# Kernel optimization log

Hardware: AMD Instinct MI355X
Metric: run time of the kernel (lower is better)

Reference implementation:

```python
import jax, jax.numpy as jnp
import numpy as np

B = 2; GH = 64; GW = 64
D = 384; H = 12; HD = D // H          # head dim 32
SD = 2                                 # spatial dims
KS = 7; ST = 3; PAD = (KS - 1) // 2    # strided conv params
RR = 0.5
NROT = (int(HD * RR) // (2 * SD)) * (2 * SD)   # 16 rotated dims per head
PAIRS = NROT // (2 * SD)                        # 4 freq pairs per spatial axis
ITERS = 3
BASE = 10000.0
LN_EPS = 1e-5
EPS = np.float32(1.1920929e-07)        # torch.finfo(float32).eps


def setup_inputs() -> dict:
    key = jax.random.key(0)
    ks = jax.random.split(key, 8)
    s = 0.02
    # base rotary frequencies with 'sqrt' scaling, per head/axis, + init jitter
    inv = BASE ** (-jnp.arange(PAIRS, dtype=jnp.float32) / PAIRS)
    inv = jnp.sqrt(inv)
    rose_freqs = jnp.broadcast_to(inv, (H, SD, PAIRS)) + 0.02 * jax.random.normal(ks[7], (H, SD, PAIRS), jnp.float32)
    return {
        "x": jax.random.normal(ks[0], (B, GH * GW, D), jnp.float32),
        "conv_w": jax.random.normal(ks[1], (D, D, KS, KS), jnp.float32) / np.float32(np.sqrt(D * KS * KS)),
        "conv_b": jnp.zeros((D,), jnp.float32),
        "kv_w": s * jax.random.normal(ks[2], (D, 2 * D), jnp.float32),
        "kv_b": jnp.zeros((2 * D,), jnp.float32),
        "q_w": s * jax.random.normal(ks[3], (D, D), jnp.float32),
        "q_b": jnp.zeros((D,), jnp.float32),
        "mlp_w1": s * jax.random.normal(ks[4], (D, 4 * D), jnp.float32),
        "mlp_b1": jnp.zeros((4 * D,), jnp.float32),
        "mlp_w2": s * jax.random.normal(ks[5], (4 * D, D), jnp.float32),
        "mlp_b2": jnp.zeros((D,), jnp.float32),
        "g1": jnp.ones((D,), jnp.float32), "b1": jnp.zeros((D,), jnp.float32),
        "g2": jnp.ones((D,), jnp.float32), "b2": jnp.zeros((D,), jnp.float32),
        "g3": jnp.ones((D,), jnp.float32), "b3": jnp.zeros((D,), jnp.float32),
        "temp": jnp.array([1.0 / np.sqrt(D)], jnp.float32),
        "rose_freqs": rose_freqs,
        "grid_h": GH,
        "grid_w": GW,
    }


def _ln(x, g, b):
    mu = jnp.mean(x, axis=-1, keepdims=True)
    var = jnp.mean(jnp.square(x - mu), axis=-1, keepdims=True)
    return (x - mu) * jax.lax.rsqrt(var + LN_EPS) * g + b


def _rose(x, freqs, grid_shape, spacing):
    """Rotary spatial embedding. x: (B, N, D) -> (B, H, N, HD) with first NROT
    head dims rotated by per-head learnable frequencies over real-space coords."""
    Bx, N, _ = x.shape
    axes = [jnp.arange(g, dtype=jnp.float32) * sp for g, sp in zip(grid_shape, spacing)]
    coords = jnp.stack(jnp.meshgrid(*axes, indexing='ij'), axis=-1).reshape(-1, SD)  # (N, SD)
    ang = jnp.einsum('ns,hsp->hnsp', coords, freqs).reshape(H, N, NROT // 2)
    cos = jnp.cos(ang)[None]; sin = jnp.sin(ang)[None]                # (1,H,N,NROT/2)
    xh = x.reshape(Bx, N, H, HD).transpose(0, 2, 1, 3)                # (B,H,N,HD)
    x1 = xh[..., 0:NROT:2]; x2 = xh[..., 1:NROT:2]
    rot = jnp.stack([x1 * cos - x2 * sin, x1 * sin + x2 * cos], axis=-1).reshape(Bx, H, N, NROT)
    return jnp.concatenate([rot, xh[..., NROT:]], axis=-1)


def reference(x, conv_w, conv_b, kv_w, kv_b, q_w, q_b, mlp_w1, mlp_b1, mlp_w2, mlp_b2,
              g1, b1, g2, b2, g3, b3, temp, rose_freqs, grid_h, grid_w):
    in_grid = (int(grid_h), int(grid_w)); in_sp = (1.0, 1.0)
    q_grid = tuple((g + 2 * PAD - KS) // ST + 1 for g in in_grid)
    q_sp = tuple(s * ST for s in in_sp)
    Bx, N_in, _ = x.shape
    N_out = q_grid[0] * q_grid[1]

    # strided conv producing low-res slots, then norm1
    xt = x.transpose(0, 2, 1).reshape(Bx, D, *in_grid)
    xo = jax.lax.conv_general_dilated(xt, conv_w, (ST, ST), [(PAD, PAD), (PAD, PAD)])
    xo = xo + conv_b[None, :, None, None]
    x_out = _ln(xo.reshape(Bx, D, N_out).transpose(0, 2, 1), g1, b1)  # (B,N_out,D)

    attn_q = attn_k = None
    for _ in range(ITERS):
        kv = x @ kv_w + kv_b
        k_lin, v = kv[..., :D], kv[..., D:]
        k = temp * _rose(k_lin, rose_freqs, in_grid, in_sp)           # (B,H,N_in,HD)
        q = _rose(x_out @ q_w + q_b, rose_freqs, q_grid, q_sp)       # (B,H,N_out,HD)
        # concrete attn: softmax over keys of q.k^T (temp already folded into k)
        attn_k = jax.nn.softmax(jnp.einsum('bhqd,bhkd->bhqk', q, k), axis=-1)
        attn_q = attn_k / (jnp.sum(attn_k, axis=-2, keepdims=True) + EPS)
        vh = v.reshape(Bx, N_in, H, HD).transpose(0, 2, 1, 3)
        upd = jnp.einsum('bhqk,bhkd->bhqd', attn_q, vh).transpose(0, 2, 1, 3).reshape(Bx, N_out, D)
        x_out = x_out + _ln(upd, g2, b2)
        h = jax.nn.gelu(x_out @ mlp_w1 + mlp_b1, approximate=False) @ mlp_w2 + mlp_b2
        x_out = x_out + _ln(h, g3, b3)
    return x_out, attn_q, attn_k
```

## Files before the change

### kernel.cpp

```cpp
#include <hip/hip_runtime.h>
#include <math.h>

#define BB 2
#define D_ 384
#define H_ 12
#define HD 32
#define NIN 4096
#define NOUT 484
#define MOUT (BB*NOUT)
#define MIN_ (BB*NIN)
#define QW_ 22
#define CK 18816
#define NSLICE 49
#define LN_EPS 1e-5f
#define EPS_ 1.1920929e-07f

typedef short bf16x8 __attribute__((ext_vector_type(8)));
typedef float f32x4  __attribute__((ext_vector_type(4)));

__device__ __forceinline__ unsigned f2bf(float f){
  unsigned u = __float_as_uint(f);
  u += 0x7fffu + ((u>>16)&1u);
  return u>>16;
}

static const size_t OXOUT = 0;
static const size_t OKB   = 371712;
static const size_t OVH   = OKB + 1572864;
static const size_t OQB   = OVH + 3145728;
static const size_t OQP   = OQB + 196608;
static const size_t OL0   = OQP + 371712;
static const size_t OCS   = OL0 + 12288;
static const size_t OLP   = OCS + 98304;
static const size_t OUPD  = OLP + 196608;
static const size_t OH1   = OUPD + 371712;
static const size_t OH2   = OH1 + 1486848;
static const size_t OQWB  = OH2 + 1486848;
static const size_t OW1B  = OQWB + 73728;
static const size_t OW2B  = OW1B + 294912;

__global__ __launch_bounds__(256)
void packxk(const float* __restrict__ x, ushort* __restrict__ xb){
  int i = blockIdx.x*256 + threadIdx.x;
  int base = i*4;
  if (base >= MIN_*D_) return;
  float4 v = *(const float4*)(x + base);
  uint2 o;
  o.x = f2bf(v.x) | (f2bf(v.y)<<16);
  o.y = f2bf(v.z) | (f2bf(v.w)<<16);
  *(uint2*)(xb + base) = o;
}

__global__ __launch_bounds__(256)
void wtk2(const float* __restrict__ cw, ushort* __restrict__ wtb){
  int i = blockIdx.x*256 + threadIdx.x;
  if (i >= CK*D_) return;
  int n = i / CK;
  int r = i - n*CK;
  int di = r/49, kyx = r - di*49;
  wtb[((size_t)kyx*D_ + n)*D_ + di] = (ushort)f2bf(cw[i]);
}

__global__ __launch_bounds__(256)
void packwk(const float* __restrict__ w, ushort* __restrict__ wb, int K, int N){
  int i = blockIdx.x*256 + threadIdx.x;
  if (i >= K*N) return;
  int k = i / N, n = i - k*N;
  wb[(size_t)n*K + k] = (ushort)f2bf(w[i]);
}

__global__ __launch_bounds__(256)
void convm(const ushort* __restrict__ xb, const ushort* __restrict__ wtb,
           float* __restrict__ part){
  __shared__ ushort As[128][40];
  __shared__ ushort Bs[128][40];
  const int t  = threadIdx.x;
  const int m0 = blockIdx.x*128, n0 = blockIdx.y*128, z = blockIdx.z;
  const int ky = z/7, kx = z - ky*7;
  const int r = t>>1, half = t&1;
  const int m = m0 + r;
  const int mq = (m < MOUT) ? m : 0;
  const int bbv = mq/NOUT, qq = mq - bbv*NOUT;
  const int oy = qq/QW_, ox = qq - oy*QW_;
  const int iy = oy*3-3+ky, ix = ox*3-3+kx;
  const bool aval = (m<MOUT) && iy>=0 && iy<64 && ix>=0 && ix<64;
  const ushort* asrc = xb + ((size_t)bbv*NIN + (aval ? iy*64+ix : 0))*D_ + half*16;
  const ushort* bsrc = wtb + ((size_t)z*D_ + n0 + r)*D_ + half*16;

  const int wv = t>>6;
  const int wr = (wv>>1)*64, wc = (wv&1)*64;
  const int ln = t&15, lq = (t>>4)&3;

  f32x4 acc[4][4];
#pragma unroll
  for (int i=0;i<4;i++)
#pragma unroll
    for (int j=0;j<4;j++) acc[i][j] = (f32x4){0.f,0.f,0.f,0.f};

  for (int dk=0; dk<D_; dk+=32){
    uint4 a0 = {0,0,0,0}, a1 = {0,0,0,0};
    if (aval){ a0 = *(const uint4*)(asrc+dk); a1 = *(const uint4*)(asrc+dk+8); }
    uint4 b0 = *(const uint4*)(bsrc+dk), b1 = *(const uint4*)(bsrc+dk+8);
    *(uint4*)&As[r][half*16]   = a0;  *(uint4*)&As[r][half*16+8] = a1;
    *(uint4*)&Bs[r][half*16]   = b0;  *(uint4*)&Bs[r][half*16+8] = b1;
    __syncthreads();
    bf16x8 af[4], bfr[4];
#pragma unroll
    for (int i=0;i<4;i++) af[i]  = *(const bf16x8*)&As[wr+i*16+ln][lq*8];
#pragma unroll
    for (int j=0;j<4;j++) bfr[j] = *(const bf16x8*)&Bs[wc+j*16+ln][lq*8];
#pragma unroll
    for (int i=0;i<4;i++)
#pragma unroll
      for (int j=0;j<4;j++)
        acc[i][j] = __builtin_amdgcn_mfma_f32_16x16x32_bf16(af[i], bfr[j], acc[i][j], 0,0,0);
    __syncthreads();
  }
#pragma unroll
  for (int i=0;i<4;i++){
    int rowb = m0 + wr + i*16 + lq*4;
#pragma unroll
    for (int j=0;j<4;j++){
      int col = n0 + wc + j*16 + ln;
#pragma unroll
      for (int rg=0; rg<4; rg++){
        int row = rowb + rg;
        if (row < MOUT) part[((size_t)z*MOUT + row)*D_ + col] = acc[i][j][rg];
      }
    }
  }
}

template<int ACT, bool ABF>
__global__ __launch_bounds__(256)
void gemmm(const void* __restrict__ Ain, const ushort* __restrict__ Wb,
           const float* __restrict__ bias, float* __restrict__ C,
           int M, int N, int K){
  __shared__ ushort As[128][40];
  __shared__ ushort Bs[128][40];
  const int t  = threadIdx.x;
  const int m0 = blockIdx.x*128, n0 = blockIdx.y*128;
  const int r = t>>1, half = t&1;
  const int m = m0 + r;
  const bool aval = (m < M);
  const float*  af32 = (const float*)Ain  + (size_t)(aval?m:0)*K + half*16;
  const ushort* ab16 = (const ushort*)Ain + (size_t)(aval?m:0)*K + half*16;
  const ushort* bsrc = Wb + (size_t)(n0 + r)*K + half*16;

  const int wv = t>>6;
  const int wr = (wv>>1)*64, wc = (wv&1)*64;
  const int ln = t&15, lq = (t>>4)&3;

  f32x4 acc[4][4];
#pragma unroll
  for (int i=0;i<4;i++)
#pragma unroll
    for (int j=0;j<4;j++) acc[i][j] = (f32x4){0.f,0.f,0.f,0.f};

  for (int dk=0; dk<K; dk+=32){
    uint4 a0 = {0,0,0,0}, a1 = {0,0,0,0};
    if (aval){
      if (ABF){
        a0 = *(const uint4*)(ab16+dk); a1 = *(const uint4*)(ab16+dk+8);
      } else {
        float4 f0 = *(const float4*)(af32+dk),   f1 = *(const float4*)(af32+dk+4);
        float4 f2 = *(const float4*)(af32+dk+8), f3 = *(const float4*)(af32+dk+12);
        a0.x = f2bf(f0.x)|(f2bf(f0.y)<<16); a0.y = f2bf(f0.z)|(f2bf(f0.w)<<16);
        a0.z = f2bf(f1.x)|(f2bf(f1.y)<<16); a0.w = f2bf(f1.z)|(f2bf(f1.w)<<16);
        a1.x = f2bf(f2.x)|(f2bf(f2.y)<<16); a1.y = f2bf(f2.z)|(f2bf(f2.w)<<16);
        a1.z = f2bf(f3.x)|(f2bf(f3.y)<<16); a1.w = f2bf(f3.z)|(f2bf(f3.w)<<16);
      }
    }
    uint4 b0 = *(const uint4*)(bsrc+dk), b1 = *(const uint4*)(bsrc+dk+8);
    *(uint4*)&As[r][half*16]   = a0;  *(uint4*)&As[r][half*16+8] = a1;
    *(uint4*)&Bs[r][half*16]   = b0;  *(uint4*)&Bs[r][half*16+8] = b1;
    __syncthreads();
    bf16x8 af[4], bfr[4];
#pragma unroll
    for (int i=0;i<4;i++) af[i]  = *(const bf16x8*)&As[wr+i*16+ln][lq*8];
#pragma unroll
    for (int j=0;j<4;j++) bfr[j] = *(const bf16x8*)&Bs[wc+j*16+ln][lq*8];
#pragma unroll
    for (int i=0;i<4;i++)
#pragma unroll
      for (int j=0;j<4;j++)
        acc[i][j] = __builtin_amdgcn_mfma_f32_16x16x32_bf16(af[i], bfr[j], acc[i][j], 0,0,0);
    __syncthreads();
  }
#pragma unroll
  for (int i=0;i<4;i++){
    int rowb = m0 + wr + i*16 + lq*4;
#pragma unroll
    for (int j=0;j<4;j++){
      int col = n0 + wc + j*16 + ln;
      float bv = bias[col];
#pragma unroll
      for (int rg=0; rg<4; rg++){
        int row = rowb + rg;
        if (row < M){
          float v = acc[i][j][rg] + bv;
          if (ACT==1) v = 0.5f*v*(1.f + erff(v*0.7071067811865475f));
          C[(size_t)row*N + col] = v;
        }
      }
    }
  }
}

__global__ __launch_bounds__(256)
void gemmsk(const float* __restrict__ Ain, const ushort* __restrict__ Wb,
            float* __restrict__ part){
  __shared__ ushort As[128][40];
  __shared__ ushort Bs[128][40];
  const int t  = threadIdx.x;
  const int m0 = blockIdx.x*128, n0 = blockIdx.y*128, z = blockIdx.z;
  const int r = t>>1, half = t&1;
  const int m = m0 + r;
  const bool aval = (m < MOUT);
  const float*  af32 = Ain + (size_t)(aval?m:0)*1536 + z*384 + half*16;
  const ushort* bsrc = Wb + (size_t)(n0 + r)*1536 + z*384 + half*16;

  const int wv = t>>6;
  const int wr = (wv>>1)*64, wc = (wv&1)*64;
  const int ln = t&15, lq = (t>>4)&3;

  f32x4 acc[4][4];
#pragma unroll
  for (int i=0;i<4;i++)
#pragma unroll
    for (int j=0;j<4;j++) acc[i][j] = (f32x4){0.f,0.f,0.f,0.f};

  for (int dk=0; dk<384; dk+=32){
    uint4 a0 = {0,0,0,0}, a1 = {0,0,0,0};
    if (aval){
      float4 f0 = *(const float4*)(af32+dk),   f1 = *(const float4*)(af32+dk+4);
      float4 f2 = *(const float4*)(af32+dk+8), f3 = *(const float4*)(af32+dk+12);
      a0.x = f2bf(f0.x)|(f2bf(f0.y)<<16); a0.y = f2bf(f0.z)|(f2bf(f0.w)<<16);
      a0.z = f2bf(f1.x)|(f2bf(f1.y)<<16); a0.w = f2bf(f1.z)|(f2bf(f1.w)<<16);
      a1.x = f2bf(f2.x)|(f2bf(f2.y)<<16); a1.y = f2bf(f2.z)|(f2bf(f2.w)<<16);
      a1.z = f2bf(f3.x)|(f2bf(f3.y)<<16); a1.w = f2bf(f3.z)|(f2bf(f3.w)<<16);
    }
    uint4 b0 = *(const uint4*)(bsrc+dk), b1 = *(const uint4*)(bsrc+dk+8);
    *(uint4*)&As[r][half*16]   = a0;  *(uint4*)&As[r][half*16+8] = a1;
    *(uint4*)&Bs[r][half*16]   = b0;  *(uint4*)&Bs[r][half*16+8] = b1;
    __syncthreads();
    bf16x8 af[4], bfr[4];
#pragma unroll
    for (int i=0;i<4;i++) af[i]  = *(const bf16x8*)&As[wr+i*16+ln][lq*8];
#pragma unroll
    for (int j=0;j<4;j++) bfr[j] = *(const bf16x8*)&Bs[wc+j*16+ln][lq*8];
#pragma unroll
    for (int i=0;i<4;i++)
#pragma unroll
      for (int j=0;j<4;j++)
        acc[i][j] = __builtin_amdgcn_mfma_f32_16x16x32_bf16(af[i], bfr[j], acc[i][j], 0,0,0);
    __syncthreads();
  }
#pragma unroll
  for (int i=0;i<4;i++){
    int rowb = m0 + wr + i*16 + lq*4;
#pragma unroll
    for (int j=0;j<4;j++){
      int col = n0 + wc + j*16 + ln;
#pragma unroll
      for (int rg=0; rg<4; rg++){
        int row = rowb + rg;
        if (row < MOUT) part[((size_t)z*MOUT + row)*D_ + col] = acc[i][j][rg];
      }
    }
  }
}

__device__ __forceinline__ float block_sum_384(float v){
  __shared__ float red[6];
#pragma unroll
  for (int o=32;o>0;o>>=1) v += __shfl_down(v,o);
  const int lane = threadIdx.x & 63, w = threadIdx.x >> 6;
  __syncthreads();
  if (lane==0) red[w] = v;
  __syncthreads();
  return red[0]+red[1]+red[2]+red[3]+red[4]+red[5];
}

template<int MODE>
__global__ __launch_bounds__(384)
void lnk(const float* __restrict__ in, const float* __restrict__ cb,
         const float* __restrict__ gg, const float* __restrict__ bb,
         float* __restrict__ xout){
  const int m = blockIdx.x, d = threadIdx.x;
  float v;
  if (MODE==0){
    v = cb[d];
    for (int z=0; z<NSLICE; z++) v += in[((size_t)z*MOUT + m)*D_ + d];
  } else if (MODE==1){
    int b = m/NOUT, q = m - b*NOUT;
    int h = d>>5, dd2 = d&31;
    v = in[(((size_t)(b*H_ + h))*NOUT + q)*HD + dd2];
  } else if (MODE==2){
    v = in[(size_t)m*D_ + d];
  } else {
    v = cb[d];
#pragma unroll
    for (int z=0; z<4; z++) v += in[((size_t)z*MOUT + m)*D_ + d];
  }
  float mu  = block_sum_384(v) * (1.f/D_);
  float ce  = v - mu;
  float var = block_sum_384(ce*ce) * (1.f/D_);
  float o = ce * rsqrtf(var + LN_EPS) * gg[d] + bb[d];
  float* dst = xout + (size_t)m*D_ + d;
  if (MODE==0) *dst = o;
  else *dst += o;
}

__global__ __launch_bounds__(256)
void rosek(const float* __restrict__ kvbuf, const float* __restrict__ rf,
           const float* __restrict__ temp,
           ushort* __restrict__ kb, float* __restrict__ vhb){
  int idx = blockIdx.x*256 + threadIdx.x;
  if (idx >= BB*H_*NIN) return;
  int n  = idx & (NIN-1);
  int bh = idx >> 12;
  int h  = bh % H_;
  int b  = bh / H_;
  float T = temp[0];
  int iy = n >> 6, ix = n & 63;
  const float* src = kvbuf + ((size_t)b*NIN + n)*768 + h*HD;
  float xv[HD];
#pragma unroll
  for (int d4=0; d4<8; d4++){
    float4 v = *(const float4*)(src + d4*4);
    xv[d4*4]=v.x; xv[d4*4+1]=v.y; xv[d4*4+2]=v.z; xv[d4*4+3]=v.w;
  }
  float out[HD];
#pragma unroll
  for (int tp=0; tp<8; tp++){
    int s2 = tp >> 2, p2 = tp & 3;
    float coord = (s2==0) ? (float)iy : (float)ix;
    float ang = coord * rf[(h*2+s2)*4 + p2];
    float sn, cn; sincosf(ang, &sn, &cn);
    float x1 = xv[2*tp], x2 = xv[2*tp+1];
    out[2*tp]   = x1*cn - x2*sn;
    out[2*tp+1] = x1*sn + x2*cn;
  }
#pragma unroll
  for (int d=16; d<HD; d++) out[d] = xv[d];
  ushort* dk = kb + ((size_t)bh*NIN + n)*HD;
#pragma unroll
  for (int g=0; g<4; g++){
    uint4 o;
    o.x = f2bf(T*out[g*8+0]) | (f2bf(T*out[g*8+1])<<16);
    o.y = f2bf(T*out[g*8+2]) | (f2bf(T*out[g*8+3])<<16);
    o.z = f2bf(T*out[g*8+4]) | (f2bf(T*out[g*8+5])<<16);
    o.w = f2bf(T*out[g*8+6]) | (f2bf(T*out[g*8+7])<<16);
    *(uint4*)(dk + g*8) = o;
  }
  const float* vs = src + D_;
  float* dv = vhb + ((size_t)bh*NIN + n)*HD;
#pragma unroll
  for (int d4=0; d4<8; d4++)
    *(float4*)(dv + d4*4) = *(const float4*)(vs + d4*4);
}

__global__ __launch_bounds__(256)
void roseq(const float* __restrict__ qp, const float* __restrict__ rf,
           ushort* __restrict__ qb){
  int idx = blockIdx.x*256 + threadIdx.x;
  int q  = idx & 511;
  int bh = idx >> 9;
  int h  = bh % H_;
  int b  = bh / H_;
  ushort* dq = qb + ((size_t)bh*512 + q)*HD;
  if (q >= NOUT){
    uint4 z = {0,0,0,0};
#pragma unroll
    for (int g=0; g<4; g++) *(uint4*)(dq + g*8) = z;
    return;
  }
  int oy = q / QW_, ox = q - oy*QW_;
  const float* src = qp + ((size_t)b*NOUT + q)*D_ + h*HD;
  float xv[HD];
#pragma unroll
  for (int d4=0; d4<8; d4++){
    float4 v = *(const float4*)(src + d4*4);
    xv[d4*4]=v.x; xv[d4*4+1]=v.y; xv[d4*4+2]=v.z; xv[d4*4+3]=v.w;
  }
  float out[HD];
#pragma unroll
  for (int tp=0; tp<8; tp++){
    int s2 = tp >> 2, p2 = tp & 3;
    float coord = (s2==0) ? 3.0f*(float)oy : 3.0f*(float)ox;
    float ang = coord * rf[(h*2+s2)*4 + p2];
    float sn, cn; sincosf(ang, &sn, &cn);
    float x1 = xv[2*tp], x2 = xv[2*tp+1];
    out[2*tp]   = x1*cn - x2*sn;
    out[2*tp+1] = x1*sn + x2*cn;
  }
#pragma unroll
  for (int d=16; d<HD; d++) out[d] = xv[d];
#pragma unroll
  for (int g=0; g<4; g++){
    uint4 o;
    o.x = f2bf(out[g*8+0]) | (f2bf(out[g*8+1])<<16);
    o.y = f2bf(out[g*8+2]) | (f2bf(out[g*8+3])<<16);
    o.z = f2bf(out[g*8+4]) | (f2bf(out[g*8+5])<<16);
    o.w = f2bf(out[g*8+6]) | (f2bf(out[g*8+7])<<16);
    *(uint4*)(dq + g*8) = o;
  }
}

__global__ __launch_bounds__(256)
void rowk(const ushort* __restrict__ qb, const ushort* __restrict__ kb,
          float* __restrict__ l0part){
  __shared__ ushort Qs[64][40];
  __shared__ ushort Ks[256][40];
  __shared__ float  red[4][64];
  const int t  = threadIdx.x;
  const int q0 = blockIdx.x*64;
  const int kt = blockIdx.y;
  const int k0 = kt*256;
  const int bh = blockIdx.z;
  {
    int row = t>>2, seg = t&3;
    const ushort* src = qb + ((size_t)bh*512 + q0 + row)*HD + seg*8;
    *(uint4*)&Qs[row][seg*8] = *(const uint4*)src;
  }
  {
    const ushort* src = kb + ((size_t)bh*NIN + k0 + t)*HD;
#pragma unroll
    for (int g=0; g<4; g++)
      *(uint4*)&Ks[t][g*8] = *(const uint4*)(src + g*8);
  }
  __syncthreads();
  const int wv = t>>6;
  const int wc = wv*64;
  const int ln = t&15, lq = (t>>4)&3;
  bf16x8 af[4], bfr[4];
#pragma unroll
  for (int i=0;i<4;i++) af[i]  = *(const bf16x8*)&Qs[i*16+ln][lq*8];
#pragma unroll
  for (int j=0;j<4;j++) bfr[j] = *(const bf16x8*)&Ks[wc+j*16+ln][lq*8];
  f32x4 acc[4][4];
  const f32x4 zero = (f32x4){0.f,0.f,0.f,0.f};
#pragma unroll
  for (int i=0;i<4;i++)
#pragma unroll
    for (int j=0;j<4;j++)
      acc[i][j] = __builtin_amdgcn_mfma_f32_16x16x32_bf16(af[i], bfr[j], zero, 0,0,0);
  float rs[4][4];
#pragma unroll
  for (int i=0;i<4;i++){
#pragma unroll
    for (int rg=0; rg<4; rg++){
      float s = 0.f;
#pragma unroll
      for (int j=0;j<4;j++) s += __expf(acc[i][j][rg]);
      rs[i][rg] = s;
    }
  }
#pragma unroll
  for (int i=0;i<4;i++)
#pragma unroll
    for (int rg=0;rg<4;rg++){
      float v = rs[i][rg];
      v += __shfl_xor(v,1); v += __shfl_xor(v,2);
      v += __shfl_xor(v,4); v += __shfl_xor(v,8);
      rs[i][rg] = v;
    }
  if (ln==0){
#pragma unroll
    for (int i=0;i<4;i++)
#pragma unroll
      for (int rg=0;rg<4;rg++)
        red[wv][i*16+lq*4+rg] = rs[i][rg];
  }
  __syncthreads();
  if (t < 64){
    float tot = red[0][t]+red[1][t]+red[2][t]+red[3][t];
    l0part[((size_t)bh*512 + q0 + t)*16 + kt] = tot;
  }
}

__global__ __launch_bounds__(256)
void l0red(const float* __restrict__ lp, float* __restrict__ l0inv){
  int i = blockIdx.x*256 + threadIdx.x;
  const float4* p = (const float4*)(lp + (size_t)i*16);
  float4 a=p[0], b=p[1], c=p[2], d=p[3];
  float s = a.x+a.y+a.z+a.w + b.x+b.y+b.z+b.w + c.x+c.y+c.z+c.w + d.x+d.y+d.z+d.w;
  l0inv[i] = 1.f/s;
}

__global__ __launch_bounds__(256)
void colk_f(const ushort* __restrict__ qb, const ushort* __restrict__ kb,
            const float* __restrict__ l0inv, float* __restrict__ csinv){
  __shared__ ushort Ks[256][40];
  __shared__ ushort Qs[64][40];
  __shared__ float  lis[64];
  const int t  = threadIdx.x;
  const int k0 = blockIdx.x*256;
  const int bh = blockIdx.y;
  {
    const ushort* src = kb + ((size_t)bh*NIN + k0 + t)*HD;
#pragma unroll
    for (int g=0; g<4; g++)
      *(uint4*)&Ks[t][g*8] = *(const uint4*)(src + g*8);
  }
  const int wv = t>>6, ln = t&15, lq = (t>>4)&3;
  const f32x4 zero = (f32x4){0.f,0.f,0.f,0.f};
  f32x4 colacc[4];
#pragma unroll
  for (int i=0;i<4;i++) colacc[i] = zero;
  for (int qc=0; qc<512; qc+=64){
    __syncthreads();
    {
      int row = t>>2, seg = t&3;
      *(uint4*)&Qs[row][seg*8] =
        *(const uint4*)(qb + ((size_t)bh*512 + qc + row)*HD + seg*8);
    }
    if (t < 64){
      int q = qc + t;
      lis[t] = (q < NOUT) ? l0inv[(size_t)bh*512 + q] : 0.f;
    }
    __syncthreads();
    bf16x8 af[4], bfr[4];
#pragma unroll
    for (int i=0;i<4;i++) af[i]  = *(const bf16x8*)&Ks[wv*64+i*16+ln][lq*8];
#pragma unroll
    for (int j=0;j<4;j++) bfr[j] = *(const bf16x8*)&Qs[j*16+ln][lq*8];
#pragma unroll
    for (int j=0;j<4;j++){
      float liv = lis[j*16+ln];
#pragma unroll
      for (int i=0;i<4;i++){
        f32x4 c = __builtin_amdgcn_mfma_f32_16x16x32_bf16(af[i], bfr[j], zero, 0,0,0);
#pragma unroll
        for (int rg=0;rg<4;rg++)
          colacc[i][rg] += __expf(c[rg]) * liv;
      }
    }
  }
#pragma unroll
  for (int i=0;i<4;i++)
#pragma unroll
    for (int rg=0;rg<4;rg++){
      float v = colacc[i][rg];
      v += __shfl_xor(v,1); v += __shfl_xor(v,2);
      v += __shfl_xor(v,4); v += __shfl_xor(v,8);
      colacc[i][rg] = v;
    }
  if (ln==0){
#pragma unroll
    for (int i=0;i<4;i++){
      float4 o;
      o.x = 1.f/(colacc[i][0] + EPS_);
      o.y = 1.f/(colacc[i][1] + EPS_);
      o.z = 1.f/(colacc[i][2] + EPS_);
      o.w = 1.f/(colacc[i][3] + EPS_);
      *(float4*)(csinv + (size_t)bh*NIN + k0 + wv*64 + i*16 + lq*4) = o;
    }
  }
}

template<bool LAST>
__global__ __launch_bounds__(256)
void pv_f(const ushort* __restrict__ qb, const ushort* __restrict__ kb,
          const float* __restrict__ vh, const float* __restrict__ l0inv,
          const float* __restrict__ csinv, float* __restrict__ upd,
          float* __restrict__ attnq, float* __restrict__ attnk){
  __shared__ ushort   Qs[32][40];
  __shared__ float    Ps[128][36];
  __shared__ unsigned Vt[32][132];
  __shared__ float    lis[32];
  __shared__ float    cis[128];
  const int t  = threadIdx.x;
  const int q0 = blockIdx.x*32;
  const int bh = blockIdx.y;
  {
    int row = t>>3, seg = t&7;
    *(uint2*)&Qs[row][seg*4] =
      *(const uint2*)(qb + ((size_t)bh*512 + q0 + row)*HD + seg*4);
  }
  if (t < 32){
    int q = q0 + t;
    lis[t] = (q < NOUT) ? l0inv[(size_t)bh*512 + q] : 0.f;
  }
  __syncthreads();
  const int wv = t>>6, ln = t&15, lq = (t>>4)&3;
  const bf16x8 af0 = *(const bf16x8*)&Qs[ln][lq*8];
  const bf16x8 af1 = *(const bf16x8*)&Qs[16+ln][lq*8];
  float lr[2][4];
#pragma unroll
  for (int i=0;i<2;i++)
#pragma unroll
    for (int rg=0;rg<4;rg++) lr[i][rg] = lis[i*16 + lq*4 + rg];
  const f32x4 zero = (f32x4){0.f,0.f,0.f,0.f};
  f32x4 acc[2][2];
  acc[0][0]=zero; acc[0][1]=zero; acc[1][0]=zero; acc[1][1]=zero;
  const ushort* kfrag = kb + ((size_t)bh*NIN)*HD;
  for (int kc=0; kc<NIN; kc+=128){
    if (LAST) __syncthreads();
    {
      int r = t>>1, half = t&1;
      float civ = csinv[(size_t)bh*NIN + kc + r];
      if (half==0) cis[r] = civ;
      const float* pv = vh + ((size_t)bh*NIN + kc + r)*HD + half*16;
      float4 b0=*(const float4*)pv, b1=*(const float4*)(pv+4),
             b2=*(const float4*)(pv+8), b3=*(const float4*)(pv+12);
      float w[16] = {civ*b0.x, civ*b0.y, civ*b0.z, civ*b0.w,
                     civ*b1.x, civ*b1.y, civ*b1.z, civ*b1.w,
                     civ*b2.x, civ*b2.y, civ*b2.z, civ*b2.w,
                     civ*b3.x, civ*b3.y, civ*b3.z, civ*b3.w};
      int dbase = half*16;
#pragma unroll
      for (int i2=0;i2<16;i2++){
        unsigned hi = f2bf(w[i2]);
        float hif = __uint_as_float(hi<<16);
        unsigned lo = f2bf(w[i2] - hif);
        Vt[dbase+i2][r] = (hi<<16) | lo;
      }
    }
    bf16x8 bf0 = *(const bf16x8*)(kfrag + (size_t)(kc + wv*32 +      ln)*HD + lq*8);
    bf16x8 bf1 = *(const bf16x8*)(kfrag + (size_t)(kc + wv*32 + 16 + ln)*HD + lq*8);
    {
      f32x4 c; float4 pw;
      c = __builtin_amdgcn_mfma_f32_16x16x32_bf16(af0, bf0, zero, 0,0,0);
      pw.x=__expf(c[0])*lr[0][0]; pw.y=__expf(c[1])*lr[0][1];
      pw.z=__expf(c[2])*lr[0][2]; pw.w=__expf(c[3])*lr[0][3];
      *(float4*)&Ps[wv*32 +      ln][      lq*4] = pw;
      c = __builtin_amdgcn_mfma_f32_16x16x32_bf16(af1, bf0, zero, 0,0,0);
      pw.x=__expf(c[0])*lr[1][0]; pw.y=__expf(c[1])*lr[1][1];
      pw.z=__expf(c[2])*lr[1][2]; pw.w=__expf(c[3])*lr[1][3];
      *(float4*)&Ps[wv*32 +      ln][16 + lq*4] = pw;
      c = __builtin_amdgcn_mfma_f32_16x16x32_bf16(af0, bf1, zero, 0,0,0);
      pw.x=__expf(c[0])*lr[0][0]; pw.y=__expf(c[1])*lr[0][1];
      pw.z=__expf(c[2])*lr[0][2]; pw.w=__expf(c[3])*lr[0][3];
      *(float4*)&Ps[wv*32 + 16 + ln][      lq*4] = pw;
      c = __builtin_amdgcn_mfma_f32_16x16x32_bf16(af1, bf1, zero, 0,0,0);
      pw.x=__expf(c[0])*lr[1][0]; pw.y=__expf(c[1])*lr[1][1];
      pw.z=__expf(c[2])*lr[1][2]; pw.w=__expf(c[3])*lr[1][3];
      *(float4*)&Ps[wv*32 + 16 + ln][16 + lq*4] = pw;
    }
    if (LAST){
      __syncthreads();
      int row = t>>3, seg = t&7;
      int q = q0 + row;
      if (q < NOUT){
        float* ak = attnk + ((size_t)bh*NOUT + q)*NIN + kc + seg*16;
        float* aq = attnq + ((size_t)bh*NOUT + q)*NIN + kc + seg*16;
#pragma unroll
        for (int s=0;s<4;s++){
          int kk = seg*16 + s*4;
          float4 p = make_float4(Ps[kk][row], Ps[kk+1][row], Ps[kk+2][row], Ps[kk+3][row]);
          float4 c4 = *(const float4*)&cis[kk];
          *(float4*)(ak + s*4) = p;
          float4 pq;
          pq.x = p.x*c4.x; pq.y = p.y*c4.y; pq.z = p.z*c4.z; pq.w = p.w*c4.w;
          *(float4*)(aq + s*4) = pq;
        }
      }
    }
    bf16x8 bhi[2], blo[2];
#pragma unroll
    for (int nf=0;nf<2;nf++){
#pragma unroll
      for (int j=0;j<8;j++){
        float p = Ps[wv*32 + lq*8 + j][nf*16 + ln];
        unsigned hi = f2bf(p);
        float hif = __uint_as_float(hi<<16);
        unsigned lo = f2bf(p - hif);
        bhi[nf][j] = (short)hi;
        blo[nf][j] = (short)lo;
      }
    }
    bf16x8 ahi[2], alo[2];
#pragma unroll
    for (int mf=0;mf<2;mf++){
      const unsigned* vrow = &Vt[mf*16+ln][wv*32 + lq*8];
      uint4 wa = *(const uint4*)vrow;
      uint4 wb = *(const uint4*)(vrow+4);
      ahi[mf][0]=(short)(wa.x>>16); alo[mf][0]=(short)(wa.x&0xffffu);
      ahi[mf][1]=(short)(wa.y>>16); alo[mf][1]=(short)(wa.y&0xffffu);
      ahi[mf][2]=(short)(wa.z>>16); alo[mf][2]=(short)(wa.z&0xffffu);
      ahi[mf][3]=(short)(wa.w>>16); alo[mf][3]=(short)(wa.w&0xffffu);
      ahi[mf][4]=(short)(wb.x>>16); alo[mf][4]=(short)(wb.x&0xffffu);
      ahi[mf][5]=(short)(wb.y>>16); alo[mf][5]=(short)(wb.y&0xffffu);
      ahi[mf][6]=(short)(wb.z>>16); alo[mf][6]=(short)(wb.z&0xffffu);
      ahi[mf][7]=(short)(wb.w>>16); alo[mf][7]=(short)(wb.w&0xffffu);
    }
#pragma unroll
    for (int mf=0;mf<2;mf++)
#pragma unroll
      for (int nf=0;nf<2;nf++){
        acc[mf][nf] = __builtin_amdgcn_mfma_f32_16x16x32_bf16(ahi[mf], bhi[nf], acc[mf][nf], 0,0,0);
        acc[mf][nf] = __builtin_amdgcn_mfma_f32_16x16x32_bf16(ahi[mf], blo[nf], acc[mf][nf], 0,0,0);
        acc[mf][nf] = __builtin_amdgcn_mfma_f32_16x16x32_bf16(alo[mf], bhi[nf], acc[mf][nf], 0,0,0);
      }
  }
  __syncthreads();
  float* Ured = &Ps[0][0];
  {
    int lane = t & 63;
#pragma unroll
    for (int mf=0;mf<2;mf++)
#pragma unroll
      for (int nf=0;nf<2;nf++)
#pragma unroll
        for (int rg=0;rg<4;rg++)
          Ured[wv*1024 + (mf*2+nf)*256 + rg*64 + lane] = acc[mf][nf][rg];
  }
  __syncthreads();
#pragma unroll
  for (int i=0;i<4;i++){
    int s = i*256 + t;
    float u = Ured[s] + Ured[1024+s] + Ured[2048+s] + Ured[3072+s];
    int grp = s>>8, rg = (s>>6)&3, lane = s&63;
    int mf = grp>>1, nf = grp&1;
    int q = q0 + nf*16 + (lane&15);
    int d = mf*16 + (lane>>4)*4 + rg;
    if (q < NOUT) upd[((size_t)bh*NOUT + q)*HD + d] = u;
  }
}

__global__ __launch_bounds__(256)
void copyk(const float* __restrict__ src, float* __restrict__ dst, int n){
  int i = blockIdx.x*256 + threadIdx.x;
  if (i < n) dst[i] = src[i];
}

extern "C" void kernel_launch(void* const* d_in, const int* in_sizes, int n_in,
                              void* d_out, int out_size, void* d_ws, size_t ws_size,
                              hipStream_t stream){
  (void)in_sizes; (void)n_in; (void)out_size; (void)ws_size;
  const float* px    = (const float*)d_in[0];
  const float* pcw   = (const float*)d_in[1];
  const float* pcb   = (const float*)d_in[2];
  const float* pkvw  = (const float*)d_in[3];
  const float* pkvb  = (const float*)d_in[4];
  const float* pqw   = (const float*)d_in[5];
  const float* pqb   = (const float*)d_in[6];
  const float* pw1   = (const float*)d_in[7];
  const float* pb1   = (const float*)d_in[8];
  const float* pw2   = (const float*)d_in[9];
  const float* pb2   = (const float*)d_in[10];
  const float* pg1   = (const float*)d_in[11];
  const float* pbe1  = (const float*)d_in[12];
  const float* pg2   = (const float*)d_in[13];
  const float* pbe2  = (const float*)d_in[14];
  const float* pg3   = (const float*)d_in[15];
  const float* pbe3  = (const float*)d_in[16];
  const float* ptemp = (const float*)d_in[17];
  const float* prf   = (const float*)d_in[18];

  float* out = (float*)d_out;
  float* ws  = (float*)d_ws;

  float* xout   = ws + OXOUT;
  ushort* kb    = (ushort*)(ws + OKB);
  float* vhb    = ws + OVH;
  ushort* qb    = (ushort*)(ws + OQB);
  float* qp     = ws + OQP;
  float* l0inv  = ws + OL0;
  float* csinv  = ws + OCS;
  float* l0part = ws + OLP;
  float* updb   = ws + OUPD;
  float* h1     = ws + OH1;
  float* h2p    = ws + OH2;
  ushort* qwb   = (ushort*)(ws + OQWB);
  ushort* w1b   = (ushort*)(ws + OW1B);
  ushort* w2b   = (ushort*)(ws + OW2B);

  float* attnq = out + 371712;
  float* attnk = out + 371712 + 47579136;
  float* kvbuf = attnq;
  float* cpart = attnq + 8388608;
  ushort* wtb  = (ushort*)attnk;
  ushort* xb16 = (ushort*)(attnk + 3612672);
  ushort* kvwb = (ushort*)(attnk + 3612672 + 1572864);

  packxk<<<dim3((MIN_*D_/4 + 255)/256), 256, 0, stream>>>(px, xb16);
  wtk2  <<<dim3((CK*D_ + 255)/256), 256, 0, stream>>>(pcw, wtb);
  packwk<<<dim3((384*768 + 255)/256), 256, 0, stream>>>(pkvw, kvwb, 384, 768);
  packwk<<<dim3((384*384 + 255)/256), 256, 0, stream>>>(pqw,  qwb,  384, 384);
  packwk<<<dim3((384*1536 + 255)/256), 256, 0, stream>>>(pw1, w1b, 384, 1536);
  packwk<<<dim3((1536*384 + 255)/256), 256, 0, stream>>>(pw2, w2b, 1536, 384);

  convm<<<dim3(8,3,NSLICE), 256, 0, stream>>>(xb16, wtb, cpart);
  lnk<0><<<dim3(MOUT), 384, 0, stream>>>(cpart, pcb, pg1, pbe1, xout);
  gemmm<0,true><<<dim3(64,6), 256, 0, stream>>>(xb16, kvwb, pkvb, kvbuf, MIN_, 768, 384);
  rosek<<<dim3((BB*H_*NIN+255)/256), 256, 0, stream>>>(kvbuf, prf, ptemp, kb, vhb);

  for (int it=0; it<3; ++it){
    gemmm<0,false><<<dim3(8,3), 256, 0, stream>>>(xout, qwb, pqb, qp, MOUT, 384, 384);
    roseq<<<dim3(48), 256, 0, stream>>>(qp, prf, qb);
    rowk<<<dim3(8,16,24), 256, 0, stream>>>(qb, kb, l0part);
    l0red<<<dim3(48), 256, 0, stream>>>(l0part, l0inv);
    colk_f<<<dim3(16,24), 256, 0, stream>>>(qb, kb, l0inv, csinv);
    if (it==2){
      pv_f<true ><<<dim3(16,24), 256, 0, stream>>>(qb, kb, vhb, l0inv, csinv, updb, attnq, attnk);
    } else {
      pv_f<false><<<dim3(16,24), 256, 0, stream>>>(qb, kb, vhb, l0inv, csinv, updb, attnq, attnk);
    }
    lnk<1><<<dim3(MOUT), 384, 0, stream>>>(updb, pcb, pg2, pbe2, xout);
    gemmm<1,false><<<dim3(8,12), 256, 0, stream>>>(xout, w1b, pb1, h1, MOUT, 1536, 384);
    gemmsk<<<dim3(8,3,4), 256, 0, stream>>>(h1, w2b, h2p);
    lnk<3><<<dim3(MOUT), 384, 0, stream>>>(h2p, pb2, pg3, pbe3, xout);
  }

  copyk<<<dim3((371712+255)/256), 256, 0, stream>>>(xout, out, 371712);
}
```

Measured before the change: 1.171 ms.

## Merge pack kernels, fold l0 reduction into consumers, use 64x64 GEMM tiles

The six weight and input pack kernels become one launch that dispatches on block index. The separate l0red launch is removed: colk_f and pv_f now sum the 16 row partials and take the reciprocal themselves. The small q-projection, MLP1 and split-K MLP2 GEMMs switch from 128x128 tiles to 64x64 tiles, giving roughly four times as many blocks for the 968-row matrices. The cost is fewer launches and better CU fill, paid for with less data reuse per tile and the l0 partial reduction being repeated in two kernels.

```diff
diff --git a/kernel.cpp b/kernel.cpp
--- a/kernel.cpp
+++ b/kernel.cpp
@@ -40,33 +40,43 @@
 static const size_t OW2B  = OW1B + 294912;
 
 __global__ __launch_bounds__(256)
-void packxk(const float* __restrict__ x, ushort* __restrict__ xb){
-  int i = blockIdx.x*256 + threadIdx.x;
-  int base = i*4;
-  if (base >= MIN_*D_) return;
-  float4 v = *(const float4*)(x + base);
-  uint2 o;
-  o.x = f2bf(v.x) | (f2bf(v.y)<<16);
-  o.y = f2bf(v.z) | (f2bf(v.w)<<16);
-  *(uint2*)(xb + base) = o;
-}
-
-__global__ __launch_bounds__(256)
-void wtk2(const float* __restrict__ cw, ushort* __restrict__ wtb){
-  int i = blockIdx.x*256 + threadIdx.x;
-  if (i >= CK*D_) return;
-  int n = i / CK;
-  int r = i - n*CK;
-  int di = r/49, kyx = r - di*49;
-  wtb[((size_t)kyx*D_ + n)*D_ + di] = (ushort)f2bf(cw[i]);
-}
-
-__global__ __launch_bounds__(256)
-void packwk(const float* __restrict__ w, ushort* __restrict__ wb, int K, int N){
-  int i = blockIdx.x*256 + threadIdx.x;
-  if (i >= K*N) return;
-  int k = i / N, n = i - k*N;
-  wb[(size_t)n*K + k] = (ushort)f2bf(w[i]);
+void packall(const float* __restrict__ px,  ushort* __restrict__ xb,
+             const float* __restrict__ cw,  ushort* __restrict__ wtb,
+             const float* __restrict__ wkv, ushort* __restrict__ kvwb,
+             const float* __restrict__ wq,  ushort* __restrict__ qwb,
+             const float* __restrict__ w1,  ushort* __restrict__ w1b,
+             const float* __restrict__ w2,  ushort* __restrict__ w2b){
+  const int bid = blockIdx.x, t = threadIdx.x;
+  if (bid < 3072){
+    int base = (bid*256 + t)*4;
+    float4 v = *(const float4*)(px + base);
+    uint2 o;
+    o.x = f2bf(v.x) | (f2bf(v.y)<<16);
+    o.y = f2bf(v.z) | (f2bf(v.w)<<16);
+    *(uint2*)(xb + base) = o;
+  } else if (bid < 31296){
+    int i = (bid-3072)*256 + t;
+    int n = i / CK;
+    int r = i - n*CK;
+    int di = r/49, kyx = r - di*49;
+    wtb[((size_t)kyx*D_ + n)*D_ + di] = (ushort)f2bf(cw[i]);
+  } else if (bid < 32448){
+    int i = (bid-31296)*256 + t;
+    int k = i/768, n = i - k*768;
+    kvwb[(size_t)n*384 + k] = (ushort)f2bf(wkv[i]);
+  } else if (bid < 33024){
+    int i = (bid-32448)*256 + t;
+    int k = i/384, n = i - k*384;
+    qwb[(size_t)n*384 + k] = (ushort)f2bf(wq[i]);
+  } else if (bid < 35328){
+    int i = (bid-33024)*256 + t;
+    int k = i/1536, n = i - k*1536;
+    w1b[(size_t)n*384 + k] = (ushort)f2bf(w1[i]);
+  } else {
+    int i = (bid-35328)*256 + t;
+    int k = i/384, n = i - k*384;
+    w2b[(size_t)n*1536 + k] = (ushort)f2bf(w2[i]);
+  }
 }
 
 __global__ __launch_bounds__(256)
@@ -207,60 +217,121 @@
   }
 }
 
-__global__ __launch_bounds__(256)
-void gemmsk(const float* __restrict__ Ain, const ushort* __restrict__ Wb,
-            float* __restrict__ part){
-  __shared__ ushort As[128][40];
-  __shared__ ushort Bs[128][40];
+template<int ACT>
+__global__ __launch_bounds__(256)
+void gemm64(const float* __restrict__ Ain, const ushort* __restrict__ Wb,
+            const float* __restrict__ bias, float* __restrict__ C,
+            int M, int N, int K){
+  __shared__ ushort As[64][40];
+  __shared__ ushort Bs[64][40];
   const int t  = threadIdx.x;
-  const int m0 = blockIdx.x*128, n0 = blockIdx.y*128, z = blockIdx.z;
-  const int r = t>>1, half = t&1;
+  const int m0 = blockIdx.x*64, n0 = blockIdx.y*64;
+  const int r = t>>2, seg = t&3;
+  const int m = m0 + r;
+  const bool aval = (m < M);
+  const float*  asrc = Ain + (size_t)(aval?m:0)*K + seg*8;
+  const ushort* bsrc = Wb + (size_t)(n0 + r)*K + seg*8;
+
+  const int wv = t>>6;
+  const int wr = (wv>>1)*32, wc = (wv&1)*32;
+  const int ln = t&15, lq = (t>>4)&3;
+
+  f32x4 acc[2][2];
+  acc[0][0]=(f32x4){0,0,0,0}; acc[0][1]=(f32x4){0,0,0,0};
+  acc[1][0]=(f32x4){0,0,0,0}; acc[1][1]=(f32x4){0,0,0,0};
+
+  for (int dk=0; dk<K; dk+=32){
+    uint4 a0 = {0,0,0,0};
+    if (aval){
+      float4 f0 = *(const float4*)(asrc+dk), f1 = *(const float4*)(asrc+dk+4);
+      a0.x = f2bf(f0.x)|(f2bf(f0.y)<<16); a0.y = f2bf(f0.z)|(f2bf(f0.w)<<16);
+      a0.z = f2bf(f1.x)|(f2bf(f1.y)<<16); a0.w = f2bf(f1.z)|(f2bf(f1.w)<<16);
+    }
+    uint4 b0 = *(const uint4*)(bsrc+dk);
+    *(uint4*)&As[r][seg*8] = a0;
+    *(uint4*)&Bs[r][seg*8] = b0;
+    __syncthreads();
+    bf16x8 af[2], bfr[2];
+#pragma unroll
+    for (int i=0;i<2;i++) af[i]  = *(const bf16x8*)&As[wr+i*16+ln][lq*8];
+#pragma unroll
+    for (int j=0;j<2;j++) bfr[j] = *(const bf16x8*)&Bs[wc+j*16+ln][lq*8];
+#pragma unroll
+    for (int i=0;i<2;i++)
+#pragma unroll
+      for (int j=0;j<2;j++)
+        acc[i][j] = __builtin_amdgcn_mfma_f32_16x16x32_bf16(af[i], bfr[j], acc[i][j], 0,0,0);
+    __syncthreads();
+  }
+#pragma unroll
+  for (int i=0;i<2;i++){
+    int rowb = m0 + wr + i*16 + lq*4;
+#pragma unroll
+    for (int j=0;j<2;j++){
+      int col = n0 + wc + j*16 + ln;
+      float bv = bias[col];
+#pragma unroll
+      for (int rg=0; rg<4; rg++){
+        int row = rowb + rg;
+        if (row < M){
+          float v = acc[i][j][rg] + bv;
+          if (ACT==1) v = 0.5f*v*(1.f + erff(v*0.7071067811865475f));
+          C[(size_t)row*N + col] = v;
+        }
+      }
+    }
+  }
+}
+
+__global__ __launch_bounds__(256)
+void gemm64sk(const float* __restrict__ Ain, const ushort* __restrict__ Wb,
+              float* __restrict__ part){
+  __shared__ ushort As[64][40];
+  __shared__ ushort Bs[64][40];
+  const int t  = threadIdx.x;
+  const int m0 = blockIdx.x*64, n0 = blockIdx.y*64, z = blockIdx.z;
+  const int r = t>>2, seg = t&3;
   const int m = m0 + r;
   const bool aval = (m < MOUT);
-  const float*  af32 = Ain + (size_t)(aval?m:0)*1536 + z*384 + half*16;
-  const ushort* bsrc = Wb + (size_t)(n0 + r)*1536 + z*384 + half*16;
+  const float*  asrc = Ain + (size_t)(aval?m:0)*1536 + z*384 + seg*8;
+  const ushort* bsrc = Wb + (size_t)(n0 + r)*1536 + z*384 + seg*8;
 
   const int wv = t>>6;
-  const int wr = (wv>>1)*64, wc = (wv&1)*64;
+  const int wr = (wv>>1)*32, wc = (wv&1)*32;
   const int ln = t&15, lq = (t>>4)&3;
 
-  f32x4 acc[4][4];
-#pragma unroll
-  for (int i=0;i<4;i++)
-#pragma unroll
-    for (int j=0;j<4;j++) acc[i][j] = (f32x4){0.f,0.f,0.f,0.f};
+  f32x4 acc[2][2];
+  acc[0][0]=(f32x4){0,0,0,0}; acc[0][1]=(f32x4){0,0,0,0};
+  acc[1][0]=(f32x4){0,0,0,0}; acc[1][1]=(f32x4){0,0,0,0};
 
   for (int dk=0; dk<384; dk+=32){
-    uint4 a0 = {0,0,0,0}, a1 = {0,0,0,0};
+    uint4 a0 = {0,0,0,0};
     if (aval){
-      float4 f0 = *(const float4*)(af32+dk),   f1 = *(const float4*)(af32+dk+4);
-      float4 f2 = *(const float4*)(af32+dk+8), f3 = *(const float4*)(af32+dk+12);
+      float4 f0 = *(const float4*)(asrc+dk), f1 = *(const float4*)(asrc+dk+4);
       a0.x = f2bf(f0.x)|(f2bf(f0.y)<<16); a0.y = f2bf(f0.z)|(f2bf(f0.w)<<16);
       a0.z = f2bf(f1.x)|(f2bf(f1.y)<<16); a0.w = f2bf(f1.z)|(f2bf(f1.w)<<16);
-      a1.x = f2bf(f2.x)|(f2bf(f2.y)<<16); a1.y = f2bf(f2.z)|(f2bf(f2.w)<<16);
-      a1.z = f2bf(f3.x)|(f2bf(f3.y)<<16); a1.w = f2bf(f3.z)|(f2bf(f3.w)<<16);
-    }
-    uint4 b0 = *(const uint4*)(bsrc+dk), b1 = *(const uint4*)(bsrc+dk+8);
-    *(uint4*)&As[r][half*16]   = a0;  *(uint4*)&As[r][half*16+8] = a1;
-    *(uint4*)&Bs[r][half*16]   = b0;  *(uint4*)&Bs[r][half*16+8] = b1;
-    __syncthreads();
-    bf16x8 af[4], bfr[4];
-#pragma unroll
-    for (int i=0;i<4;i++) af[i]  = *(const bf16x8*)&As[wr+i*16+ln][lq*8];
-#pragma unroll
-    for (int j=0;j<4;j++) bfr[j] = *(const bf16x8*)&Bs[wc+j*16+ln][lq*8];
-#pragma unroll
-    for (int i=0;i<4;i++)
-#pragma unroll
-      for (int j=0;j<4;j++)
+    }
+    uint4 b0 = *(const uint4*)(bsrc+dk);
+    *(uint4*)&As[r][seg*8] = a0;
+    *(uint4*)&Bs[r][seg*8] = b0;
+    __syncthreads();
+    bf16x8 af[2], bfr[2];
+#pragma unroll
+    for (int i=0;i<2;i++) af[i]  = *(const bf16x8*)&As[wr+i*16+ln][lq*8];
+#pragma unroll
+    for (int j=0;j<2;j++) bfr[j] = *(const bf16x8*)&Bs[wc+j*16+ln][lq*8];
+#pragma unroll
+    for (int i=0;i<2;i++)
+#pragma unroll
+      for (int j=0;j<2;j++)
         acc[i][j] = __builtin_amdgcn_mfma_f32_16x16x32_bf16(af[i], bfr[j], acc[i][j], 0,0,0);
     __syncthreads();
   }
 #pragma unroll
-  for (int i=0;i<4;i++){
+  for (int i=0;i<2;i++){
     int rowb = m0 + wr + i*16 + lq*4;
 #pragma unroll
-    for (int j=0;j<4;j++){
+    for (int j=0;j<2;j++){
       int col = n0 + wc + j*16 + ln;
 #pragma unroll
       for (int rg=0; rg<4; rg++){
@@ -296,8 +367,6 @@
     int b = m/NOUT, q = m - b*NOUT;
     int h = d>>5, dd2 = d&31;
     v = in[(((size_t)(b*H_ + h))*NOUT + q)*HD + dd2];
-  } else if (MODE==2){
-    v = in[(size_t)m*D_ + d];
   } else {
     v = cb[d];
 #pragma unroll
@@ -481,17 +550,8 @@
 }
 
 __global__ __launch_bounds__(256)
-void l0red(const float* __restrict__ lp, float* __restrict__ l0inv){
-  int i = blockIdx.x*256 + threadIdx.x;
-  const float4* p = (const float4*)(lp + (size_t)i*16);
-  float4 a=p[0], b=p[1], c=p[2], d=p[3];
-  float s = a.x+a.y+a.z+a.w + b.x+b.y+b.z+b.w + c.x+c.y+c.z+c.w + d.x+d.y+d.z+d.w;
-  l0inv[i] = 1.f/s;
-}
-
-__global__ __launch_bounds__(256)
 void colk_f(const ushort* __restrict__ qb, const ushort* __restrict__ kb,
-            const float* __restrict__ l0inv, float* __restrict__ csinv){
+            const float* __restrict__ l0part, float* __restrict__ csinv){
   __shared__ ushort Ks[256][40];
   __shared__ ushort Qs[64][40];
   __shared__ float  lis[64];
@@ -518,7 +578,11 @@
     }
     if (t < 64){
       int q = qc + t;
-      lis[t] = (q < NOUT) ? l0inv[(size_t)bh*512 + q] : 0.f;
+      const float* lp = l0part + ((size_t)bh*512 + q)*16;
+      float s = 0.f;
+#pragma unroll
+      for (int j=0;j<16;j++) s += lp[j];
+      lis[t] = (q < NOUT) ? 1.f/s : 0.f;
     }
     __syncthreads();
     bf16x8 af[4], bfr[4];
@@ -563,7 +627,7 @@
 template<bool LAST>
 __global__ __launch_bounds__(256)
 void pv_f(const ushort* __restrict__ qb, const ushort* __restrict__ kb,
-          const float* __restrict__ vh, const float* __restrict__ l0inv,
+          const float* __restrict__ vh, const float* __restrict__ l0part,
           const float* __restrict__ csinv, float* __restrict__ upd,
           float* __restrict__ attnq, float* __restrict__ attnk){
   __shared__ ushort   Qs[32][40];
@@ -581,7 +645,11 @@
   }
   if (t < 32){
     int q = q0 + t;
-    lis[t] = (q < NOUT) ? l0inv[(size_t)bh*512 + q] : 0.f;
+    const float* lp = l0part + ((size_t)bh*512 + q)*16;
+    float s = 0.f;
+#pragma unroll
+    for (int j=0;j<16;j++) s += lp[j];
+    lis[t] = (q < NOUT) ? 1.f/s : 0.f;
   }
   __syncthreads();
   const int wv = t>>6, ln = t&15, lq = (t>>4)&3;
@@ -758,7 +826,6 @@
   float* vhb    = ws + OVH;
   ushort* qb    = (ushort*)(ws + OQB);
   float* qp     = ws + OQP;
-  float* l0inv  = ws + OL0;
   float* csinv  = ws + OCS;
   float* l0part = ws + OLP;
   float* updb   = ws + OUPD;
@@ -776,12 +843,8 @@
   ushort* xb16 = (ushort*)(attnk + 3612672);
   ushort* kvwb = (ushort*)(attnk + 3612672 + 1572864);
 
-  packxk<<<dim3((MIN_*D_/4 + 255)/256), 256, 0, stream>>>(px, xb16);
-  wtk2  <<<dim3((CK*D_ + 255)/256), 256, 0, stream>>>(pcw, wtb);
-  packwk<<<dim3((384*768 + 255)/256), 256, 0, stream>>>(pkvw, kvwb, 384, 768);
-  packwk<<<dim3((384*384 + 255)/256), 256, 0, stream>>>(pqw,  qwb,  384, 384);
-  packwk<<<dim3((384*1536 + 255)/256), 256, 0, stream>>>(pw1, w1b, 384, 1536);
-  packwk<<<dim3((1536*384 + 255)/256), 256, 0, stream>>>(pw2, w2b, 1536, 384);
+  packall<<<dim3(37632), 256, 0, stream>>>(px, xb16, pcw, wtb, pkvw, kvwb,
+                                           pqw, qwb, pw1, w1b, pw2, w2b);
 
   convm<<<dim3(8,3,NSLICE), 256, 0, stream>>>(xb16, wtb, cpart);
   lnk<0><<<dim3(MOUT), 384, 0, stream>>>(cpart, pcb, pg1, pbe1, xout);
@@ -789,19 +852,18 @@
   rosek<<<dim3((BB*H_*NIN+255)/256), 256, 0, stream>>>(kvbuf, prf, ptemp, kb, vhb);
 
   for (int it=0; it<3; ++it){
-    gemmm<0,false><<<dim3(8,3), 256, 0, stream>>>(xout, qwb, pqb, qp, MOUT, 384, 384);
+    gemm64<0><<<dim3(16,6), 256, 0, stream>>>(xout, qwb, pqb, qp, MOUT, 384, 384);
     roseq<<<dim3(48), 256, 0, stream>>>(qp, prf, qb);
     rowk<<<dim3(8,16,24), 256, 0, stream>>>(qb, kb, l0part);
-    l0red<<<dim3(48), 256, 0, stream>>>(l0part, l0inv);
-    colk_f<<<dim3(16,24), 256, 0, stream>>>(qb, kb, l0inv, csinv);
+    colk_f<<<dim3(16,24), 256, 0, stream>>>(qb, kb, l0part, csinv);
     if (it==2){
-      pv_f<true ><<<dim3(16,24), 256, 0, stream>>>(qb, kb, vhb, l0inv, csinv, updb, attnq, attnk);
+      pv_f<true ><<<dim3(16,24), 256, 0, stream>>>(qb, kb, vhb, l0part, csinv, updb, attnq, attnk);
     } else {
-      pv_f<false><<<dim3(16,24), 256, 0, stream>>>(qb, kb, vhb, l0inv, csinv, updb, attnq, attnk);
+      pv_f<false><<<dim3(16,24), 256, 0, stream>>>(qb, kb, vhb, l0part, csinv, updb, attnq, attnk);
     }
     lnk<1><<<dim3(MOUT), 384, 0, stream>>>(updb, pcb, pg2, pbe2, xout);
-    gemmm<1,false><<<dim3(8,12), 256, 0, stream>>>(xout, w1b, pb1, h1, MOUT, 1536, 384);
-    gemmsk<<<dim3(8,3,4), 256, 0, stream>>>(h1, w2b, h2p);
+    gemm64<1><<<dim3(16,24), 256, 0, stream>>>(xout, w1b, pb1, h1, MOUT, 1536, 384);
+    gemm64sk<<<dim3(16,6,4), 256, 0, stream>>>(h1, w2b, h2p);
     lnk<3><<<dim3(MOUT), 384, 0, stream>>>(h2p, pb2, pg3, pbe3, xout);
   }
 
```

After: 1.067 ms. 1.1x faster.
